# Kernel tuning notes

Measured on AMD Instinct MI355X. Metric: run time of the kernel, lower is better.

The kernel has to match this reference:

```python
import jax, jax.numpy as jnp
import numpy as np

B, N, CQ, H, CH = 1, 256, 128, 4, 32  # batch, n_res, c_q(=c_k=c_v), heads, per-head dim


def setup_inputs() -> dict:
    key = jax.random.key(0)
    ks = jax.random.split(key, 12)
    s = 0.02
    q_x = jax.random.normal(ks[0], (B, N, N, CQ), jnp.float32)
    kv_x = jax.random.normal(ks[1], (B, N, N, CQ), jnp.float32)
    # mask bias: 0 where kept, -1e9 where masked (additive mask)
    keep = jax.random.uniform(ks[2], (B, N, 1, 1, N)) < 0.9
    mask_bias = jnp.where(keep, 0.0, -1e9).astype(jnp.float32)
    triangle_bias = jax.random.normal(ks[3], (B, 1, H, N, N), jnp.float32)
    # projection weights, stored per-head as [H, CH, C_in]
    wq = jax.random.normal(ks[4], (H, CH, CQ), jnp.float32) * s
    wk = jax.random.normal(ks[5], (H, CH, CQ), jnp.float32) * s
    wv = jax.random.normal(ks[6], (H, CH, CQ), jnp.float32) * s
    wg = jax.random.normal(ks[7], (H, CH, CQ), jnp.float32) * s
    bg = jax.random.normal(ks[8], (H, CH), jnp.float32) * s + 1.0  # gating bias init 1
    wo = jax.random.normal(ks[9], (CQ, H * CH), jnp.float32) * s
    bo = jnp.zeros((CQ,), jnp.float32)
    return {"q_x": q_x, "kv_x": kv_x, "mask_bias": mask_bias,
            "triangle_bias": triangle_bias, "wq": wq, "wk": wk, "wv": wv,
            "wg": wg, "bg": bg, "wo": wo, "bo": bo}


def reference(q_x, kv_x, mask_bias, triangle_bias, wq, wk, wv, wg, bg, wo, bo):
    scale = 1.0 / np.sqrt(CH).astype(np.float32)
    # project + split heads: [B,N,Q,C] x [H,D,C] -> [B,N,H,Q,D]
    q = jnp.einsum('bnqc,hdc->bnhqd', q_x, wq) * scale
    k = jnp.einsum('bnkc,hdc->bnhkd', kv_x, wk)
    v = jnp.einsum('bnkc,hdc->bnhkd', kv_x, wv)
    # scores + additive biases (mask_bias broadcasts over h,q; triangle over n)
    a = jnp.einsum('bnhqd,bnhkd->bnhqk', q, k) + mask_bias + triangle_bias
    a = jax.nn.softmax(a, axis=-1)
    o = jnp.einsum('bnhqk,bnhkd->bnhqd', a, v)
    o = jnp.swapaxes(o, -2, -3)  # [B,N,Q,H,D]
    # gating
    g = jax.nn.sigmoid(jnp.einsum('bnqc,hdc->bnqhd', q_x, wg) + bg)
    o = o * g
    o = o.reshape(o.shape[:-2] + (H * CH,))  # [B,N,Q,H*D]
    return jnp.einsum('bnqe,ce->bnqc', o, wo) + bo
```

## Files before the change

kernel.cpp:

```cpp
#include <hip/hip_runtime.h>

#define NRES 256
#define CIN  128
#define NH   4
#define DH   32

typedef __attribute__((ext_vector_type(4))) float f32x4;
typedef __attribute__((ext_vector_type(8))) short bf16x8;
typedef unsigned short u16;

#define U_WQG 0
#define U_WKV 32768
#define U_WWO 65536
#define U_QB  131072
#define U_KB  (U_QB + 8388608)
#define U_VT  (U_KB + 8388608)
#define U_GB  (U_VT + 8388608)
#define WS_NEED ((size_t)(U_GB + 8388608) * 2)

__device__ __forceinline__ unsigned pkbf(float a, float b) {
    unsigned ua = __builtin_bit_cast(unsigned, a);
    unsigned ub = __builtin_bit_cast(unsigned, b);
    ua += 0x7fffu + ((ua >> 16) & 1u);
    ub += 0x7fffu + ((ub >> 16) & 1u);
    return __builtin_amdgcn_perm(ub, ua, 0x07060302);
}
__device__ __forceinline__ u16 f2bfu(float f) {
    unsigned u = __builtin_bit_cast(unsigned, f);
    return (u16)((u + 0x7fffu + ((u >> 16) & 1u)) >> 16);
}
__device__ __forceinline__ float bf2f(u16 v) {
    unsigned u = ((unsigned)v) << 16;
    return __builtin_bit_cast(float, u);
}
union bfr { unsigned u[4]; bf16x8 v; };
__device__ __forceinline__ bf16x8 ldcvt8(const float* __restrict__ p) {
    f32x4 a = *(const f32x4*)p; f32x4 b = *(const f32x4*)(p + 4);
    bfr r;
    r.u[0] = pkbf(a[0], a[1]); r.u[1] = pkbf(a[2], a[3]);
    r.u[2] = pkbf(b[0], b[1]); r.u[3] = pkbf(b[2], b[3]);
    return r.v;
}
__device__ __forceinline__ bf16x8 ldcvt8s(const float* __restrict__ p, float sc) {
    f32x4 a = *(const f32x4*)p; f32x4 b = *(const f32x4*)(p + 4);
    bfr r;
    r.u[0] = pkbf(a[0] * sc, a[1] * sc); r.u[1] = pkbf(a[2] * sc, a[3] * sc);
    r.u[2] = pkbf(b[0] * sc, b[1] * sc); r.u[3] = pkbf(b[2] * sc, b[3] * sc);
    return r.v;
}
#define MFMA(a, b, c) __builtin_amdgcn_mfma_f32_16x16x32_bf16((a), (b), (c), 0, 0, 0)

__global__ void wconv(const float* __restrict__ wq, const float* __restrict__ wk,
                      const float* __restrict__ wv, const float* __restrict__ wg,
                      const float* __restrict__ wo, u16* __restrict__ ws)
{
    const int i0 = (blockIdx.x * 256 + threadIdx.x) * 8;
    const float qsc = 0.17677669529663687f;
    const float* src; u16* dst; float sc = 1.f;
    if (i0 < 32768) {
        const int e = i0 >> 7, c = i0 & 127;
        src = (e < 128 ? wq + e * CIN : wg + (e - 128) * CIN) + c;
        if (e < 128) sc = qsc;
        dst = ws + U_WQG + i0;
    } else if (i0 < 65536) {
        const int j = i0 - 32768, e = j >> 7, c = j & 127;
        src = (e < 128 ? wk + e * CIN : wv + (e - 128) * CIN) + c;
        dst = ws + U_WKV + j;
    } else {
        const int j = i0 - 65536;
        src = wo + j; dst = ws + U_WWO + j;
    }
    *(bf16x8*)dst = ldcvt8s(src, sc);
}

__global__ __launch_bounds__(256, 4) void proj(
    const float* __restrict__ q_x, const float* __restrict__ kv_x,
    const float* __restrict__ bg, u16* __restrict__ ws)
{
    const int t = threadIdx.x, lane = t & 63, w = t >> 6;
    const int mrow = lane & 15, grp = lane >> 4;
    const int koff = grp * 8, rbase = grp * 4;
    const int R0 = blockIdx.x * 64;
    const int e0 = w * 64;
    const int ysel = blockIdx.y;
    const float* __restrict__ src = ysel ? kv_x : q_x;
    const u16* __restrict__ W = ws + (ysel ? U_WKV : U_WQG);
    const bool vpath = (ysel == 1) && (w >= 2);

    const f32x4 zf = {0.f, 0.f, 0.f, 0.f};
    f32x4 acc[4][4];
    #pragma unroll
    for (int mt = 0; mt < 4; ++mt)
        #pragma unroll
        for (int nt = 0; nt < 4; ++nt) acc[mt][nt] = zf;

    if (!vpath) {
        #pragma unroll 1
        for (int ct = 0; ct < 4; ++ct) {
            const int c0 = ct * 32 + koff;
            const bf16x8 bw0 = *(const bf16x8*)(W + (e0 +  0 + mrow) * CIN + c0);
            const bf16x8 bw1 = *(const bf16x8*)(W + (e0 + 16 + mrow) * CIN + c0);
            const bf16x8 bw2 = *(const bf16x8*)(W + (e0 + 32 + mrow) * CIN + c0);
            const bf16x8 bw3 = *(const bf16x8*)(W + (e0 + 48 + mrow) * CIN + c0);
            #pragma unroll
            for (int mt = 0; mt < 4; ++mt) {
                const bf16x8 aX = ldcvt8(src + (size_t)(R0 + mt * 16 + mrow) * CIN + c0);
                acc[mt][0] = MFMA(bw0, aX, acc[mt][0]);
                acc[mt][1] = MFMA(bw1, aX, acc[mt][1]);
                acc[mt][2] = MFMA(bw2, aX, acc[mt][2]);
                acc[mt][3] = MFMA(bw3, aX, acc[mt][3]);
            }
        }
    } else {
        #pragma unroll 1
        for (int ct = 0; ct < 4; ++ct) {
            const int c0 = ct * 32 + koff;
            const bf16x8 bw0 = *(const bf16x8*)(W + (e0 +  0 + mrow) * CIN + c0);
            const bf16x8 bw1 = *(const bf16x8*)(W + (e0 + 16 + mrow) * CIN + c0);
            const bf16x8 bw2 = *(const bf16x8*)(W + (e0 + 32 + mrow) * CIN + c0);
            const bf16x8 bw3 = *(const bf16x8*)(W + (e0 + 48 + mrow) * CIN + c0);
            #pragma unroll
            for (int mt = 0; mt < 4; ++mt) {
                const bf16x8 aX = ldcvt8(src + (size_t)(R0 + mt * 16 + mrow) * CIN + c0);
                acc[mt][0] = MFMA(aX, bw0, acc[mt][0]);
                acc[mt][1] = MFMA(aX, bw1, acc[mt][1]);
                acc[mt][2] = MFMA(aX, bw2, acc[mt][2]);
                acc[mt][3] = MFMA(aX, bw3, acc[mt][3]);
            }
        }
    }

    if (!ysel) {
        if (w < 2) {
            #pragma unroll
            for (int mt = 0; mt < 4; ++mt) {
                const size_t row = (size_t)(R0 + mt * 16 + mrow);
                #pragma unroll
                for (int nt = 0; nt < 4; ++nt) {
                    uint2 v;
                    v.x = pkbf(acc[mt][nt][0], acc[mt][nt][1]);
                    v.y = pkbf(acc[mt][nt][2], acc[mt][nt][3]);
                    *(uint2*)&ws[U_QB + row * CIN + e0 + nt * 16 + rbase] = v;
                }
            }
        } else {
            #pragma unroll
            for (int mt = 0; mt < 4; ++mt) {
                const size_t row = (size_t)(R0 + mt * 16 + mrow);
                #pragma unroll
                for (int nt = 0; nt < 4; ++nt) {
                    const int eb = (e0 - 128) + nt * 16 + rbase;
                    const f32x4 bgv = *(const f32x4*)(bg + eb);
                    float g[4];
                    #pragma unroll
                    for (int r = 0; r < 4; ++r)
                        g[r] = 1.f / (1.f + __expf(-(acc[mt][nt][r] + bgv[r])));
                    uint2 v;
                    v.x = pkbf(g[0], g[1]);
                    v.y = pkbf(g[2], g[3]);
                    *(uint2*)&ws[U_GB + row * CIN + eb] = v;
                }
            }
        }
    } else {
        if (w < 2) {
            #pragma unroll
            for (int mt = 0; mt < 4; ++mt) {
                const size_t row = (size_t)(R0 + mt * 16 + mrow);
                #pragma unroll
                for (int nt = 0; nt < 4; ++nt) {
                    uint2 v;
                    v.x = pkbf(acc[mt][nt][0], acc[mt][nt][1]);
                    v.y = pkbf(acc[mt][nt][2], acc[mt][nt][3]);
                    *(uint2*)&ws[U_KB + row * CIN + e0 + nt * 16 + rbase] = v;
                }
            }
        } else {
            const int n = R0 >> 8;
            #pragma unroll
            for (int mt = 0; mt < 4; ++mt) {
                const int k0 = (R0 & 255) + mt * 16 + rbase;
                #pragma unroll
                for (int nt = 0; nt < 4; ++nt) {
                    const int d = (e0 - 128) + nt * 16 + mrow;
                    uint2 v;
                    v.x = pkbf(acc[mt][nt][0], acc[mt][nt][1]);
                    v.y = pkbf(acc[mt][nt][2], acc[mt][nt][3]);
                    *(uint2*)&ws[U_VT + ((size_t)n * 128 + d) * 256 + k0] = v;
                }
            }
        }
    }
}

#define PST 40
__global__ __launch_bounds__(256, 4) void flash(
    u16* __restrict__ ws, const float* __restrict__ mask_bias,
    const float* __restrict__ tri_bias)
{
    const int h = blockIdx.x, n = blockIdx.y;
    const int t = threadIdx.x, lane = t & 63, w = t >> 6;
    const int mrow = lane & 15, grp = lane >> 4;
    const int koff = grp * 8, rbase = grp * 4;
    const int q0 = w * 64;

    __shared__ u16 Pt[4 * 64 * PST];
    __shared__ float msk[NRES];

    if (t < 64) *(float4*)&msk[t * 4] = *(const float4*)(mask_bias + n * NRES + t * 4);

    u16* __restrict__ QOg = ws + U_QB + (size_t)n * NRES * CIN;
    const u16* __restrict__ Kb = ws + U_KB + (size_t)n * NRES * CIN;
    const u16* __restrict__ Vt = ws + U_VT + (size_t)n * 128 * 256;
    const u16* __restrict__ Gb = ws + U_GB + (size_t)n * NRES * CIN;
    const float* __restrict__ trih = tri_bias + (size_t)h * NRES * NRES;

    bf16x8 aq[4];
    #pragma unroll
    for (int qt = 0; qt < 4; ++qt)
        aq[qt] = *(const bf16x8*)(QOg + (size_t)(q0 + qt * 16 + mrow) * CIN + h * DH + koff);
    __syncthreads();

    const f32x4 zf = {0.f, 0.f, 0.f, 0.f};
    f32x4 oa[4][2];
    float ls[4];
    #pragma unroll
    for (int qt = 0; qt < 4; ++qt) { oa[qt][0] = zf; oa[qt][1] = zf; ls[qt] = 0.f; }

    u16* __restrict__ pw = &Pt[w * 64 * PST];

    for (int kt = 0; kt < 8; ++kt) {
        const int kb = kt * 32;
        bf16x8 bk0 = *(const bf16x8*)(Kb + (size_t)(kb + mrow) * CIN + h * DH + koff);
        bf16x8 bk1 = *(const bf16x8*)(Kb + (size_t)(kb + 16 + mrow) * CIN + h * DH + koff);
        bf16x8 bv0 = *(const bf16x8*)(Vt + (size_t)(h * DH + mrow) * NRES + kb + koff);
        bf16x8 bv1 = *(const bf16x8*)(Vt + (size_t)(h * DH + 16 + mrow) * NRES + kb + koff);
        const f32x4 m0 = *(const f32x4*)&msk[kb + rbase];
        const f32x4 m1 = *(const f32x4*)&msk[kb + 16 + rbase];

        #pragma unroll
        for (int qt = 0; qt < 4; ++qt) {
            const int q = q0 + qt * 16 + mrow;
            const f32x4 t0 = *(const f32x4*)(trih + (size_t)q * NRES + kb + rbase);
            const f32x4 t1 = *(const f32x4*)(trih + (size_t)q * NRES + kb + 16 + rbase);
            f32x4 s0 = MFMA(bk0, aq[qt], zf);
            f32x4 s1 = MFMA(bk1, aq[qt], zf);
            float part = 0.f;
            #pragma unroll
            for (int r = 0; r < 4; ++r) {
                s0[r] = __expf(s0[r] + t0[r] + m0[r] - 8.f);
                s1[r] = __expf(s1[r] + t1[r] + m1[r] - 8.f);
                part += s0[r] + s1[r];
            }
            ls[qt] += part;
            uint2 v0, v1;
            v0.x = pkbf(s0[0], s0[1]); v0.y = pkbf(s0[2], s0[3]);
            v1.x = pkbf(s1[0], s1[1]); v1.y = pkbf(s1[2], s1[3]);
            *(uint2*)&pw[(qt * 16 + mrow) * PST + rbase]      = v0;
            *(uint2*)&pw[(qt * 16 + mrow) * PST + 16 + rbase] = v1;
        }
        asm volatile("s_waitcnt lgkmcnt(0)" ::: "memory");
        __builtin_amdgcn_sched_barrier(0);
        #pragma unroll
        for (int qt = 0; qt < 4; ++qt) {
            bf16x8 pa = *(const bf16x8*)&pw[(qt * 16 + mrow) * PST + koff];
            oa[qt][0] = MFMA(bv0, pa, oa[qt][0]);
            oa[qt][1] = MFMA(bv1, pa, oa[qt][1]);
        }
    }

    #pragma unroll
    for (int qt = 0; qt < 4; ++qt) {
        float lv = ls[qt];
        lv += __shfl_xor(lv, 16, 64);
        lv += __shfl_xor(lv, 32, 64);
        const float inv = 1.f / lv;
        const int q = q0 + qt * 16 + mrow;
        #pragma unroll
        for (int half = 0; half < 2; ++half) {
            const size_t off = (size_t)q * CIN + h * DH + half * 16 + rbase;
            const uint2 gv = *(const uint2*)&Gb[off];
            const float g0 = bf2f((u16)(gv.x)),        g1 = bf2f((u16)(gv.x >> 16));
            const float g2 = bf2f((u16)(gv.y)),        g3 = bf2f((u16)(gv.y >> 16));
            uint2 ov;
            ov.x = pkbf(oa[qt][half][0] * inv * g0, oa[qt][half][1] * inv * g1);
            ov.y = pkbf(oa[qt][half][2] * inv * g2, oa[qt][half][3] * inv * g3);
            *(uint2*)&QOg[off] = ov;
        }
    }
}

__global__ __launch_bounds__(256, 4) void gout(
    const u16* __restrict__ ws, const float* __restrict__ bo,
    float* __restrict__ out)
{
    const int t = threadIdx.x, lane = t & 63, w = t >> 6;
    const int mrow = lane & 15, grp = lane >> 4;
    const int koff = grp * 8, rbase = grp * 4;
    const int r0 = blockIdx.x * 128 + w * 32;
    const u16* __restrict__ Wo = ws + U_WWO;
    const u16* __restrict__ QOg = ws + U_QB;

    const f32x4 zf = {0.f, 0.f, 0.f, 0.f};
    f32x4 acc[2][8];
    #pragma unroll
    for (int at = 0; at < 2; ++at)
        #pragma unroll
        for (int nt = 0; nt < 8; ++nt) acc[at][nt] = zf;

    #pragma unroll
    for (int ks = 0; ks < 4; ++ks) {
        const int e0 = ks * 32 + koff;
        const bf16x8 a0 = *(const bf16x8*)(QOg + (size_t)(r0 + mrow) * CIN + e0);
        const bf16x8 a1 = *(const bf16x8*)(QOg + (size_t)(r0 + 16 + mrow) * CIN + e0);
        #pragma unroll
        for (int nt = 0; nt < 8; ++nt) {
            const bf16x8 bw = *(const bf16x8*)(Wo + (nt * 16 + mrow) * CIN + e0);
            acc[0][nt] = MFMA(bw, a0, acc[0][nt]);
            acc[1][nt] = MFMA(bw, a1, acc[1][nt]);
        }
    }

    #pragma unroll
    for (int nt = 0; nt < 8; ++nt) {
        const f32x4 bov = *(const f32x4*)&bo[nt * 16 + rbase];
        #pragma unroll
        for (int at = 0; at < 2; ++at) {
            const f32x4 v = acc[at][nt] + bov;
            *(f32x4*)&out[(size_t)(r0 + at * 16 + mrow) * CIN + nt * 16 + rbase] = v;
        }
    }
}

#define KST 32
#define VST 264
#define GST 136

__global__ __launch_bounds__(256, 3) void attn_fb(
    const float* __restrict__ q_x, const float* __restrict__ kv_x,
    const float* __restrict__ mask_bias, const float* __restrict__ tri_bias,
    const float* __restrict__ wq, const float* __restrict__ wk,
    const float* __restrict__ wv, float* __restrict__ o_out)
{
    const int h = blockIdx.x, n = blockIdx.y;
    const int t = threadIdx.x;
    const int lane = t & 63, w = t >> 6;
    const int mrow = lane & 15;
    const int grp  = lane >> 4;
    const int koff = grp * 8;
    const int rbase = grp * 4;
    const int q0 = w * 64;

    __shared__ u16 Ks[NRES * KST];
    __shared__ u16 Vt[DH * VST];
    __shared__ u16 Ptb[4 * 32 * PST];
    __shared__ float msk[NRES];

    if (t < 64) *(float4*)&msk[t * 4] = *(const float4*)(mask_bias + n * NRES + t * 4);

    const float* __restrict__ qxn = q_x  + (size_t)n * NRES * CIN;
    const float* __restrict__ kxn = kv_x + (size_t)n * NRES * CIN;
    const float* __restrict__ wqh = wq + h * DH * CIN;
    const float* __restrict__ wkh = wk + h * DH * CIN;
    const float* __restrict__ wvh = wv + h * DH * CIN;

    f32x4 aq_[4][2], ak_[4][2], av_[4][2];
    const f32x4 zf = {0.f, 0.f, 0.f, 0.f};
    #pragma unroll
    for (int qt = 0; qt < 4; ++qt)
        #pragma unroll
        for (int dt = 0; dt < 2; ++dt) { aq_[qt][dt] = zf; ak_[qt][dt] = zf; av_[qt][dt] = zf; }

    const float qsc = 0.17677669529663687f;
    #pragma unroll
    for (int ct = 0; ct < 4; ++ct) {
        const int c0 = ct * 32 + koff;
        bf16x8 bq0 = ldcvt8s(wqh + mrow * CIN + c0, qsc);
        bf16x8 bq1 = ldcvt8s(wqh + (16 + mrow) * CIN + c0, qsc);
        bf16x8 bk0 = ldcvt8(wkh + mrow * CIN + c0);
        bf16x8 bk1 = ldcvt8(wkh + (16 + mrow) * CIN + c0);
        bf16x8 bv0 = ldcvt8(wvh + mrow * CIN + c0);
        bf16x8 bv1 = ldcvt8(wvh + (16 + mrow) * CIN + c0);
        #pragma unroll
        for (int qt = 0; qt < 4; ++qt) {
            bf16x8 aX = ldcvt8(qxn + (q0 + qt * 16 + mrow) * CIN + c0);
            aq_[qt][0] = MFMA(aX, bq0, aq_[qt][0]);
            aq_[qt][1] = MFMA(aX, bq1, aq_[qt][1]);
            bf16x8 aK = ldcvt8(kxn + (q0 + qt * 16 + mrow) * CIN + c0);
            ak_[qt][0] = MFMA(aK, bk0, ak_[qt][0]);
            ak_[qt][1] = MFMA(aK, bk1, ak_[qt][1]);
            av_[qt][0] = MFMA(aK, bv0, av_[qt][0]);
            av_[qt][1] = MFMA(aK, bv1, av_[qt][1]);
        }
    }

    #pragma unroll
    for (int qt = 0; qt < 4; ++qt)
        #pragma unroll
        for (int dt = 0; dt < 2; ++dt)
            #pragma unroll
            for (int r = 0; r < 4; ++r) {
                const int row = q0 + qt * 16 + rbase + r;
                const int d = dt * 16 + mrow;
                Ks[row * KST + d] = f2bfu(ak_[qt][dt][r]);
                Vt[d * VST + row] = f2bfu(av_[qt][dt][r]);
            }

    u16* __restrict__ pw = &Ptb[w * 32 * PST];
    bf16x8 aq[4];
    #pragma unroll
    for (int h2 = 0; h2 < 2; ++h2) {
        #pragma unroll
        for (int j = 0; j < 2; ++j) {
            const int qt = h2 * 2 + j;
            #pragma unroll
            for (int dt = 0; dt < 2; ++dt)
                #pragma unroll
                for (int r = 0; r < 4; ++r)
                    pw[(j * 16 + rbase + r) * PST + dt * 16 + mrow] = f2bfu(aq_[qt][dt][r]);
        }
        asm volatile("s_waitcnt lgkmcnt(0)" ::: "memory");
        #pragma unroll
        for (int j = 0; j < 2; ++j)
            aq[h2 * 2 + j] = *(const bf16x8*)&pw[(j * 16 + mrow) * PST + koff];
        asm volatile("s_waitcnt lgkmcnt(0)" ::: "memory");
    }
    __syncthreads();

    f32x4 oa[4][2], ls4[4];
    #pragma unroll
    for (int qt = 0; qt < 4; ++qt) { oa[qt][0] = zf; oa[qt][1] = zf; ls4[qt] = zf; }

    const float* __restrict__ trih = tri_bias + (size_t)h * NRES * NRES;

    for (int kt = 0; kt < 8; ++kt) {
        const int kb = kt * 32;
        bf16x8 bk0 = *(const bf16x8*)&Ks[(kb + mrow) * KST + koff];
        bf16x8 bk1 = *(const bf16x8*)&Ks[(kb + 16 + mrow) * KST + koff];
        bf16x8 bv0 = *(const bf16x8*)&Vt[mrow * VST + kb + koff];
        bf16x8 bv1 = *(const bf16x8*)&Vt[(16 + mrow) * VST + kb + koff];
        const float mb0 = msk[kb + mrow] - 8.f;
        const float mb1 = msk[kb + 16 + mrow] - 8.f;

        #pragma unroll
        for (int h2 = 0; h2 < 2; ++h2) {
            float tr0[2][4], tr1[2][4];
            #pragma unroll
            for (int j = 0; j < 2; ++j) {
                const int qt = h2 * 2 + j;
                const float* __restrict__ trow =
                    trih + (q0 + qt * 16 + rbase) * NRES + kb + mrow;
                #pragma unroll
                for (int r = 0; r < 4; ++r) {
                    tr0[j][r] = trow[r * NRES];
                    tr1[j][r] = trow[r * NRES + 16];
                }
            }
            #pragma unroll
            for (int j = 0; j < 2; ++j) {
                const int qt = h2 * 2 + j;
                f32x4 s0 = MFMA(aq[qt], bk0, zf);
                f32x4 s1 = MFMA(aq[qt], bk1, zf);
                #pragma unroll
                for (int r = 0; r < 4; ++r) {
                    s0[r] = __expf(s0[r] + tr0[j][r] + mb0);
                    s1[r] = __expf(s1[r] + tr1[j][r] + mb1);
                }
                ls4[qt] += s0 + s1;
                #pragma unroll
                for (int r = 0; r < 4; ++r) {
                    pw[(j * 16 + rbase + r) * PST + mrow]      = f2bfu(s0[r]);
                    pw[(j * 16 + rbase + r) * PST + 16 + mrow] = f2bfu(s1[r]);
                }
            }
            asm volatile("s_waitcnt lgkmcnt(0)" ::: "memory");
            #pragma unroll
            for (int j = 0; j < 2; ++j) {
                const int qt = h2 * 2 + j;
                bf16x8 pa = *(const bf16x8*)&pw[(j * 16 + mrow) * PST + koff];
                oa[qt][0] = MFMA(pa, bv0, oa[qt][0]);
                oa[qt][1] = MFMA(pa, bv1, oa[qt][1]);
            }
        }
    }

    float* __restrict__ orow = o_out + (size_t)n * NRES * CIN + h * DH;
    #pragma unroll
    for (int qt = 0; qt < 4; ++qt) {
        f32x4 lv = ls4[qt];
        #pragma unroll
        for (int xm = 1; xm < 16; xm <<= 1) {
            lv[0] += __shfl_xor(lv[0], xm, 64);
            lv[1] += __shfl_xor(lv[1], xm, 64);
            lv[2] += __shfl_xor(lv[2], xm, 64);
            lv[3] += __shfl_xor(lv[3], xm, 64);
        }
        #pragma unroll
        for (int r = 0; r < 4; ++r) {
            const float inv = 1.f / lv[r];
            const int q = q0 + qt * 16 + rbase + r;
            orow[q * CIN + mrow]      = oa[qt][0][r] * inv;
            orow[q * CIN + 16 + mrow] = oa[qt][1][r] * inv;
        }
    }
}

__global__ __launch_bounds__(256, 4) void gate_fb(
    const float* __restrict__ q_x, const float* __restrict__ wg,
    const float* __restrict__ bg, const float* __restrict__ wo,
    const float* __restrict__ bo, float* io)
{
    const int t = threadIdx.x;
    const int lane = t & 63, w = t >> 6;
    const int mrow = lane & 15, grp = lane >> 4;
    const int koff = grp * 8, rbase = grp * 4;
    const int r0 = blockIdx.x * 128 + w * 32;

    __shared__ u16 Gt[4 * 32 * GST];
    u16* __restrict__ gw = &Gt[w * 32 * GST];

    const f32x4 zf = {0.f, 0.f, 0.f, 0.f};
    f32x4 acc[2][8];
    #pragma unroll
    for (int at = 0; at < 2; ++at)
        #pragma unroll
        for (int nt = 0; nt < 8; ++nt) acc[at][nt] = zf;

    #pragma unroll
    for (int ks = 0; ks < 4; ++ks) {
        const int c0 = ks * 32 + koff;
        bf16x8 ax0 = ldcvt8(q_x + (size_t)(r0 + mrow) * CIN + c0);
        bf16x8 ax1 = ldcvt8(q_x + (size_t)(r0 + 16 + mrow) * CIN + c0);
        #pragma unroll
        for (int nt = 0; nt < 8; ++nt) {
            bf16x8 bw = ldcvt8(wg + (nt * 16 + mrow) * CIN + c0);
            acc[0][nt] = MFMA(ax0, bw, acc[0][nt]);
            acc[1][nt] = MFMA(ax1, bw, acc[1][nt]);
        }
    }

    #pragma unroll
    for (int nt = 0; nt < 8; ++nt) {
        const float bge = bg[nt * 16 + mrow];
        #pragma unroll
        for (int at = 0; at < 2; ++at)
            #pragma unroll
            for (int r = 0; r < 4; ++r) {
                const int qg = r0 + at * 16 + rbase + r;
                const float ov = io[(size_t)qg * CIN + nt * 16 + mrow];
                const float g = 1.f / (1.f + __expf(-(acc[at][nt][r] + bge)));
                gw[(at * 16 + rbase + r) * GST + nt * 16 + mrow] = f2bfu(ov * g);
            }
    }
    asm volatile("s_waitcnt lgkmcnt(0)" ::: "memory");

    f32x4 acc2[2][8];
    #pragma unroll
    for (int at = 0; at < 2; ++at)
        #pragma unroll
        for (int nt = 0; nt < 8; ++nt) acc2[at][nt] = zf;

    #pragma unroll
    for (int ks = 0; ks < 4; ++ks) {
        const int e0 = ks * 32 + koff;
        bf16x8 ag0 = *(const bf16x8*)&gw[mrow * GST + e0];
        bf16x8 ag1 = *(const bf16x8*)&gw[(16 + mrow) * GST + e0];
        #pragma unroll
        for (int nt = 0; nt < 8; ++nt) {
            bf16x8 bw = ldcvt8(wo + (nt * 16 + mrow) * CIN + e0);
            acc2[0][nt] = MFMA(ag0, bw, acc2[0][nt]);
            acc2[1][nt] = MFMA(ag1, bw, acc2[1][nt]);
        }
    }

    #pragma unroll
    for (int nt = 0; nt < 8; ++nt) {
        const float boc = bo[nt * 16 + mrow];
        #pragma unroll
        for (int at = 0; at < 2; ++at)
            #pragma unroll
            for (int r = 0; r < 4; ++r)
                io[(size_t)(r0 + at * 16 + rbase + r) * CIN + nt * 16 + mrow] =
                    acc2[at][nt][r] + boc;
    }
}

extern "C" void kernel_launch(void* const* d_in, const int* in_sizes, int n_in,
                              void* d_out, int out_size, void* d_ws, size_t ws_size,
                              hipStream_t stream) {
    const float* q_x  = (const float*)d_in[0];
    const float* kv_x = (const float*)d_in[1];
    const float* mask = (const float*)d_in[2];
    const float* tri  = (const float*)d_in[3];
    const float* wq   = (const float*)d_in[4];
    const float* wk   = (const float*)d_in[5];
    const float* wv   = (const float*)d_in[6];
    const float* wg   = (const float*)d_in[7];
    const float* bg   = (const float*)d_in[8];
    const float* wo   = (const float*)d_in[9];
    const float* bo   = (const float*)d_in[10];
    float* out = (float*)d_out;

    if (ws_size >= WS_NEED) {
        u16* ws16 = (u16*)d_ws;
        wconv<<<40, 256, 0, stream>>>(wq, wk, wv, wg, wo, ws16);
        proj<<<dim3(1024, 2), 256, 0, stream>>>(q_x, kv_x, bg, ws16);
        flash<<<dim3(NH, NRES), 256, 0, stream>>>(ws16, mask, tri);
        gout<<<512, 256, 0, stream>>>(ws16, bo, out);
    } else {
        attn_fb<<<dim3(NH, NRES), 256, 0, stream>>>(q_x, kv_x, mask, tri, wq, wk, wv, out);
        gate_fb<<<(NRES * NRES) / 128, 256, 0, stream>>>(q_x, wg, bg, wo, bo, out);
    }
}
```

Before: 247.1 us.

## Stage input rows in LDS once per block and prefetch weight fragments

The projection kernel now loads and converts each block's 64x128 fp32 input tile to bf16 once into padded shared memory. Before, each of the four waves re-read and re-converted the same rows from global memory. The weight fragments for the next K-chunk are also prefetched into registers while the current chunk's MFMAs run. This cuts redundant global traffic and conversion work, at the cost of a block-wide barrier, more LDS and register pressure, and fewer blocks per CU (launch bound lowered from 4 to 3).

After: 225.4 us. -8.8%, faster.

```diff
diff --git a/kernel.cpp b/kernel.cpp
--- a/kernel.cpp
+++ b/kernel.cpp
@@ -73,7 +73,8 @@
     *(bf16x8*)dst = ldcvt8s(src, sc);
 }
 
-__global__ __launch_bounds__(256, 4) void proj(
+#define AST 136
+__global__ __launch_bounds__(256, 3) void proj(
     const float* __restrict__ q_x, const float* __restrict__ kv_x,
     const float* __restrict__ bg, u16* __restrict__ ws)
 {
@@ -87,46 +88,68 @@
     const u16* __restrict__ W = ws + (ysel ? U_WKV : U_WQG);
     const bool vpath = (ysel == 1) && (w >= 2);
 
+    __shared__ u16 As[64 * AST];
+
+    {
+        const int srow = w * 16 + mrow;
+        const float* __restrict__ sp = src + (size_t)(R0 + srow) * CIN + grp * 32;
+        u16* __restrict__ dp = &As[srow * AST + grp * 32];
+        #pragma unroll
+        for (int cc = 0; cc < 4; ++cc)
+            *(bf16x8*)(dp + cc * 8) = ldcvt8(sp + cc * 8);
+    }
+
     const f32x4 zf = {0.f, 0.f, 0.f, 0.f};
     f32x4 acc[4][4];
     #pragma unroll
     for (int mt = 0; mt < 4; ++mt)
         #pragma unroll
         for (int nt = 0; nt < 4; ++nt) acc[mt][nt] = zf;
+
+    bf16x8 bw0 = *(const bf16x8*)(W + (e0 +  0 + mrow) * CIN + koff);
+    bf16x8 bw1 = *(const bf16x8*)(W + (e0 + 16 + mrow) * CIN + koff);
+    bf16x8 bw2 = *(const bf16x8*)(W + (e0 + 32 + mrow) * CIN + koff);
+    bf16x8 bw3 = *(const bf16x8*)(W + (e0 + 48 + mrow) * CIN + koff);
+
+    __syncthreads();
 
     if (!vpath) {
         #pragma unroll 1
         for (int ct = 0; ct < 4; ++ct) {
+            const int c0n = ((ct + 1) & 3) * 32 + koff;
+            const bf16x8 nb0 = *(const bf16x8*)(W + (e0 +  0 + mrow) * CIN + c0n);
+            const bf16x8 nb1 = *(const bf16x8*)(W + (e0 + 16 + mrow) * CIN + c0n);
+            const bf16x8 nb2 = *(const bf16x8*)(W + (e0 + 32 + mrow) * CIN + c0n);
+            const bf16x8 nb3 = *(const bf16x8*)(W + (e0 + 48 + mrow) * CIN + c0n);
             const int c0 = ct * 32 + koff;
-            const bf16x8 bw0 = *(const bf16x8*)(W + (e0 +  0 + mrow) * CIN + c0);
-            const bf16x8 bw1 = *(const bf16x8*)(W + (e0 + 16 + mrow) * CIN + c0);
-            const bf16x8 bw2 = *(const bf16x8*)(W + (e0 + 32 + mrow) * CIN + c0);
-            const bf16x8 bw3 = *(const bf16x8*)(W + (e0 + 48 + mrow) * CIN + c0);
             #pragma unroll
             for (int mt = 0; mt < 4; ++mt) {
-                const bf16x8 aX = ldcvt8(src + (size_t)(R0 + mt * 16 + mrow) * CIN + c0);
+                const bf16x8 aX = *(const bf16x8*)&As[(mt * 16 + mrow) * AST + c0];
                 acc[mt][0] = MFMA(bw0, aX, acc[mt][0]);
                 acc[mt][1] = MFMA(bw1, aX, acc[mt][1]);
                 acc[mt][2] = MFMA(bw2, aX, acc[mt][2]);
                 acc[mt][3] = MFMA(bw3, aX, acc[mt][3]);
             }
+            bw0 = nb0; bw1 = nb1; bw2 = nb2; bw3 = nb3;
         }
     } else {
         #pragma unroll 1
         for (int ct = 0; ct < 4; ++ct) {
+            const int c0n = ((ct + 1) & 3) * 32 + koff;
+            const bf16x8 nb0 = *(const bf16x8*)(W + (e0 +  0 + mrow) * CIN + c0n);
+            const bf16x8 nb1 = *(const bf16x8*)(W + (e0 + 16 + mrow) * CIN + c0n);
+            const bf16x8 nb2 = *(const bf16x8*)(W + (e0 + 32 + mrow) * CIN + c0n);
+            const bf16x8 nb3 = *(const bf16x8*)(W + (e0 + 48 + mrow) * CIN + c0n);
             const int c0 = ct * 32 + koff;
-            const bf16x8 bw0 = *(const bf16x8*)(W + (e0 +  0 + mrow) * CIN + c0);
-            const bf16x8 bw1 = *(const bf16x8*)(W + (e0 + 16 + mrow) * CIN + c0);
-            const bf16x8 bw2 = *(const bf16x8*)(W + (e0 + 32 + mrow) * CIN + c0);
-            const bf16x8 bw3 = *(const bf16x8*)(W + (e0 + 48 + mrow) * CIN + c0);
             #pragma unroll
             for (int mt = 0; mt < 4; ++mt) {
-                const bf16x8 aX = ldcvt8(src + (size_t)(R0 + mt * 16 + mrow) * CIN + c0);
+                const bf16x8 aX = *(const bf16x8*)&As[(mt * 16 + mrow) * AST + c0];
                 acc[mt][0] = MFMA(aX, bw0, acc[mt][0]);
                 acc[mt][1] = MFMA(aX, bw1, acc[mt][1]);
                 acc[mt][2] = MFMA(aX, bw2, acc[mt][2]);
                 acc[mt][3] = MFMA(aX, bw3, acc[mt][3]);
             }
+            bw0 = nb0; bw1 = nb1; bw2 = nb2; bw3 = nb3;
         }
     }
 
```
